# Performance work log

Measured on AMD Instinct MI355X. Metric: run time of the kernel, lower is better.

The kernel has to match this reference:

```python
import jax, jax.numpy as jnp
import numpy as np

RES_DIM = 2048
LEAK_RATE = 0.2
BIAS_SCALE = 0.1


def setup_inputs() -> dict:
    key = jax.random.key(0)
    k_x, k_w, k_b, k_adj = jax.random.split(key, 4)
    x = jax.random.normal(k_x, (RES_DIM, RES_DIM), dtype=jnp.float32)
    # Stand-in for the powerlaw-structured reservoir weight (fixed buffer at runtime);
    # scale so spectral radius is O(1) like normalize_radius_to=1.
    weight = jax.random.normal(k_w, (RES_DIM, RES_DIM), dtype=jnp.float32) / jnp.sqrt(
        jnp.float32(RES_DIM))
    # bias: uniform(-1,1), mean-centered, scaled by bias_scale
    b = jax.random.uniform(k_b, (RES_DIM,), dtype=jnp.float32, minval=-1.0, maxval=1.0)
    bias = (b - b.mean()) * BIAS_SCALE
    # adjacency: random binary 0/1 matrix (np.random.randint(2, size=(D, D)))
    adjacency = (jax.random.uniform(k_adj, (RES_DIM, RES_DIM)) < 0.5).astype(jnp.float32)
    state0 = jnp.zeros((RES_DIM, RES_DIM), dtype=jnp.float32)
    return {"x": x, "weight": weight, "adjacency": adjacency, "bias": bias,
            "state0": state0, "n_steps": 64}


def reference(x, weight, adjacency, bias, state0, n_steps):
    drive = x @ weight + bias  # loop-invariant: precompute once

    def step(state, _):
        y = drive + state @ adjacency
        y = (1.0 - LEAK_RATE) * state + LEAK_RATE * jnp.tanh(y)
        return y, None

    final_state, _ = jax.lax.scan(step, state0, None, length=n_steps)
    return final_state
```

## Files before the change

kernel.cpp:

```cpp
#include <hip/hip_runtime.h>

#define DIM 2048
#define LEAK 0.2f

typedef __bf16 bf16x8 __attribute__((ext_vector_type(8)));
typedef float  f32x4  __attribute__((ext_vector_type(4)));
typedef unsigned int u32x4 __attribute__((ext_vector_type(4)));
typedef int    i32x4  __attribute__((ext_vector_type(4)));

static __device__ __forceinline__ unsigned short f2bf(float f) {
    unsigned int x = __float_as_uint(f);
    return (unsigned short)((x + 0x7fffu + ((x >> 16) & 1u)) >> 16);
}
static __device__ __forceinline__ float bf2f(unsigned short h) {
    return __uint_as_float(((unsigned int)h) << 16);
}

static __device__ __forceinline__ void async16(const void* g, void* s) {
    __builtin_amdgcn_global_load_lds(
        (const __attribute__((address_space(1))) void*)g,
        (__attribute__((address_space(3))) void*)s, 16, 0, 0);
}

static __device__ __forceinline__ bf16x8 ld_bf16_frag(const char* p) {
    union { u32x4 u; bf16x8 v; } cv;
    cv.u = *(const u32x4*)p;
    return cv.v;
}


__global__ __launch_bounds__(256) void split_kernel(
    const float* __restrict__ in,
    unsigned short* __restrict__ hi, unsigned short* __restrict__ lo) {
    int idx = blockIdx.x * 256 + threadIdx.x;
    float4 v = ((const float4*)in)[idx];
    ushort4 h, l;
    h.x = f2bf(v.x); l.x = f2bf(v.x - bf2f(h.x));
    h.y = f2bf(v.y); l.y = f2bf(v.y - bf2f(h.y));
    h.z = f2bf(v.z); l.z = f2bf(v.z - bf2f(h.z));
    h.w = f2bf(v.w); l.w = f2bf(v.w - bf2f(h.w));
    ((ushort4*)hi)[idx] = h;
    ((ushort4*)lo)[idx] = l;
}

__global__ __launch_bounds__(256) void transpose_split(
    const float* __restrict__ in,
    unsigned short* __restrict__ hiT, unsigned short* __restrict__ loT) {
    __shared__ float t[32][33];
    int bx = blockIdx.x, by = blockIdx.y;
    int tx = threadIdx.x & 31, ty4 = (threadIdx.x >> 5) << 2;
#pragma unroll
    for (int i = 0; i < 4; i++)
        t[ty4 + i][tx] = in[(size_t)(by * 32 + ty4 + i) * DIM + bx * 32 + tx];
    __syncthreads();
#pragma unroll
    for (int i = 0; i < 4; i++) {
        float v = t[tx][ty4 + i];
        size_t o = (size_t)(bx * 32 + ty4 + i) * DIM + by * 32 + tx;
        unsigned short h = f2bf(v);
        hiT[o] = h;
        loT[o] = f2bf(v - bf2f(h));
    }
}

__global__ __launch_bounds__(256) void transpose_i8(
    const float* __restrict__ in, signed char* __restrict__ outT) {
    __shared__ float t[32][33];
    int bx = blockIdx.x, by = blockIdx.y;
    int tx = threadIdx.x & 31, ty4 = (threadIdx.x >> 5) << 2;
#pragma unroll
    for (int i = 0; i < 4; i++)
        t[ty4 + i][tx] = in[(size_t)(by * 32 + ty4 + i) * DIM + bx * 32 + tx];
    __syncthreads();
#pragma unroll
    for (int i = 0; i < 4; i++)
        outT[(size_t)(bx * 32 + ty4 + i) * DIM + by * 32 + tx] =
            (signed char)t[tx][ty4 + i];
}

__global__ __launch_bounds__(256) void quant_split(
    const float* __restrict__ in,
    signed char* __restrict__ hi, signed char* __restrict__ lo) {
    int idx = blockIdx.x * 256 + threadIdx.x;
    float4 v = ((const float4*)in)[idx];
    char4 h, l;
    {
        int q = (int)rintf(v.x * 16384.f); q = q > 16383 ? 16383 : (q < -16383 ? -16383 : q);
        h.x = (signed char)(q >> 7); l.x = (signed char)(q & 127);
    }
    {
        int q = (int)rintf(v.y * 16384.f); q = q > 16383 ? 16383 : (q < -16383 ? -16383 : q);
        h.y = (signed char)(q >> 7); l.y = (signed char)(q & 127);
    }
    {
        int q = (int)rintf(v.z * 16384.f); q = q > 16383 ? 16383 : (q < -16383 ? -16383 : q);
        h.z = (signed char)(q >> 7); l.z = (signed char)(q & 127);
    }
    {
        int q = (int)rintf(v.w * 16384.f); q = q > 16383 ? 16383 : (q < -16383 ? -16383 : q);
        h.w = (signed char)(q >> 7); l.w = (signed char)(q & 127);
    }
    ((char4*)hi)[idx] = h;
    ((char4*)lo)[idx] = l;
}

template <int MODE>
__global__ __launch_bounds__(512, 2) void gemm128(
    const unsigned short* __restrict__ Ahi,
    const unsigned short* __restrict__ Alo,
    const unsigned short* __restrict__ BT,
    const float* __restrict__ Cin,
    const float* __restrict__ bias,
    float* __restrict__ Cout) {
    __shared__ alignas(16) char lds[3][49152];

    const int bid = blockIdx.x;
    const int xcd = bid & 7, slot = bid >> 3;
    const int tm = ((xcd >> 1) << 2) + (slot >> 3);
    const int tn = ((xcd & 1) << 3) + (slot & 7);
    const int row0 = tm << 7, col0 = tn << 7;

    const int tid = threadIdx.x;
    const int lane = tid & 63;
    const int quad = lane >> 4, l16 = lane & 15;
    const int wave = tid >> 6;
    const int wm = wave >> 1, wn = wave & 1;

    const unsigned short* a_src[4]; int a_dst[4];
    const unsigned short* b_src[2]; int b_dst[2];
#pragma unroll
    for (int i = 0; i < 4; i++) {
        int s = tid + 512 * i;
        int r = s >> 4, g = (s >> 3) & 1, c = (s & 7) ^ (r & 7);
        a_src[i] = (g ? Alo : Ahi) + (size_t)(row0 + r) * DIM + c * 8;
        a_dst[i] = s * 16;
    }
#pragma unroll
    for (int i = 0; i < 2; i++) {
        int s = tid + 512 * i;
        int r = s >> 3, c = (s & 7) ^ (r & 7);
        b_src[i] = BT + (size_t)(col0 + r) * DIM + c * 8;
        b_dst[i] = s * 16;
    }

    int aoff[2][2], boff[4][2];
#pragma unroll
    for (int i = 0; i < 2; i++)
#pragma unroll
        for (int kk = 0; kk < 2; kk++) {
            const int r = (wm << 5) + (i << 4) + l16;
            const int cs = ((kk << 2) + quad) ^ (r & 7);
            aoff[i][kk] = ((r << 4) + cs) * 16;
        }
#pragma unroll
    for (int j = 0; j < 4; j++)
#pragma unroll
        for (int kk = 0; kk < 2; kk++) {
            const int r = (wn << 6) + (j << 4) + l16;
            const int cs = ((kk << 2) + quad) ^ (r & 7);
            boff[j][kk] = ((r << 3) + cs) * 16;
        }

    f32x4 acc[2][4] = {};

    auto stage6 = [&](char* base, int k0) {
#pragma unroll
        for (int i = 0; i < 4; i++) async16(a_src[i] + k0, base + a_dst[i]);
#pragma unroll
        for (int i = 0; i < 2; i++) async16(b_src[i] + k0, base + 32768 + b_dst[i]);
    };

    stage6(lds[0], 0);
    stage6(lds[1], 64);
    asm volatile("s_waitcnt vmcnt(6)" ::: "memory");

    for (int t = 0; t < 32; ++t) {
        const char* A = lds[t % 3];
        const char* B = A + 32768;

        __builtin_amdgcn_s_barrier();
        __builtin_amdgcn_sched_barrier(0);
        if (t + 2 < 32) stage6(lds[(t + 2) % 3], (t + 2) << 6);

        bf16x8 ah[2][2], al[2][2], bv[4][2];
#pragma unroll
        for (int i = 0; i < 2; i++)
#pragma unroll
            for (int kk = 0; kk < 2; kk++) {
                ah[i][kk] = ld_bf16_frag(A + aoff[i][kk]);
                al[i][kk] = ld_bf16_frag(A + aoff[i][kk] + 128);
            }
#pragma unroll
        for (int j = 0; j < 4; j++)
#pragma unroll
            for (int kk = 0; kk < 2; kk++)
                bv[j][kk] = ld_bf16_frag(B + boff[j][kk]);

        __builtin_amdgcn_s_setprio(1);
#pragma unroll
        for (int i = 0; i < 2; i++)
#pragma unroll
            for (int j = 0; j < 4; j++)
#pragma unroll
                for (int kk = 0; kk < 2; kk++) {
                    acc[i][j] = __builtin_amdgcn_mfma_f32_16x16x32_bf16(ah[i][kk], bv[j][kk], acc[i][j], 0, 0, 0);
                    acc[i][j] = __builtin_amdgcn_mfma_f32_16x16x32_bf16(al[i][kk], bv[j][kk], acc[i][j], 0, 0, 0);
                }
        __builtin_amdgcn_s_setprio(0);

        __builtin_amdgcn_sched_barrier(0);
        if (t < 30)       asm volatile("s_waitcnt vmcnt(6)" ::: "memory");
        else if (t == 30) asm volatile("s_waitcnt vmcnt(0)" ::: "memory");
    }

#pragma unroll
    for (int i = 0; i < 2; i++) {
        const int rb = row0 + (wm << 5) + (i << 4) + (quad << 2);
#pragma unroll
        for (int j = 0; j < 4; j++) {
            const int c = col0 + (wn << 6) + (j << 4) + l16;
#pragma unroll
            for (int g = 0; g < 4; g++) {
                const size_t idx = (size_t)(rb + g) * DIM + c;
                if (MODE == 0) Cout[idx] = acc[i][j][g];
                else           Cout[idx] = Cin[idx] + acc[i][j][g] + bias[c];
            }
        }
    }
}

__global__ __launch_bounds__(512, 2) void step_i8(
    const signed char* __restrict__ Ah,
    const signed char* __restrict__ Al,
    const signed char* __restrict__ BT,
    const float* __restrict__ drive,
    float* __restrict__ out,
    signed char* __restrict__ Oh,
    signed char* __restrict__ Ol,
    int write_f32) {
    __shared__ alignas(16) char lds[3][49152];

    const int bid = blockIdx.x;
    const int xcd = bid & 7, slot = bid >> 3;
    const int tm = ((xcd >> 1) << 2) + (slot >> 3);
    const int tn = ((xcd & 1) << 3) + (slot & 7);
    const int row0 = tm << 7, col0 = tn << 7;

    const int tid = threadIdx.x;
    const int lane = tid & 63;
    const int quad = lane >> 4, l16 = lane & 15;
    const int wave = tid >> 6;
    const int wm = wave >> 1;
    const int wn = wave & 1;

    const signed char* a_src[4]; int a_dst[4];
    const signed char* b_src[2]; int b_dst[2];
#pragma unroll
    for (int i = 0; i < 4; i++) {
        int s = tid + 512 * i;
        int r = s >> 4, g = (s >> 3) & 1, c = (s & 7) ^ (r & 7);
        a_src[i] = (g ? Al : Ah) + (size_t)(row0 + r) * DIM + c * 16;
        a_dst[i] = s * 16;
    }
#pragma unroll
    for (int i = 0; i < 2; i++) {
        int s = tid + 512 * i;
        int r = s >> 3, c = (s & 7) ^ (r & 7);
        b_src[i] = BT + (size_t)(col0 + r) * DIM + c * 16;
        b_dst[i] = s * 16;
    }

    int aoff[2][2], boff[4][2];
#pragma unroll
    for (int i = 0; i < 2; i++)
#pragma unroll
        for (int kk = 0; kk < 2; kk++) {
            const int r = (wm << 5) + (i << 4) + l16;
            const int cs = ((kk << 2) + quad) ^ (r & 7);
            aoff[i][kk] = ((r << 4) + cs) * 16;
        }
#pragma unroll
    for (int j = 0; j < 4; j++)
#pragma unroll
        for (int kk = 0; kk < 2; kk++) {
            const int r = (wn << 6) + (j << 4) + l16;
            const int cs = ((kk << 2) + quad) ^ (r & 7);
            boff[j][kk] = ((r << 3) + cs) * 16;
        }

    i32x4 acch[2][4] = {};
    i32x4 accl[2][4] = {};
    float dreg[2][4][4];

    auto stage6 = [&](char* base, int k0) {
#pragma unroll
        for (int i = 0; i < 4; i++) async16(a_src[i] + k0, base + a_dst[i]);
#pragma unroll
        for (int i = 0; i < 2; i++) async16(b_src[i] + k0, base + 32768 + b_dst[i]);
    };

    stage6(lds[0], 0);
    stage6(lds[1], 128);
    asm volatile("s_waitcnt vmcnt(6)" ::: "memory");

    for (int t = 0; t < 16; ++t) {
        const char* A = lds[t % 3];
        const char* B = A + 32768;

        __builtin_amdgcn_s_barrier();
        __builtin_amdgcn_sched_barrier(0);
        if (t + 2 < 16) stage6(lds[(t + 2) % 3], (t + 2) << 7);

        if (t == 15) {
#pragma unroll
            for (int i = 0; i < 2; i++) {
                const int rb = row0 + (wm << 5) + (i << 4) + (quad << 2);
#pragma unroll
                for (int j = 0; j < 4; j++) {
                    const int c = col0 + (wn << 6) + (j << 4) + l16;
#pragma unroll
                    for (int g = 0; g < 4; g++)
                        dreg[i][j][g] = drive[(size_t)(rb + g) * DIM + c];
                }
            }
        }

        i32x4 ah[2][2], al[2][2], bv[4][2];
#pragma unroll
        for (int i = 0; i < 2; i++)
#pragma unroll
            for (int kk = 0; kk < 2; kk++) {
                ah[i][kk] = *(const i32x4*)(A + aoff[i][kk]);
                al[i][kk] = *(const i32x4*)(A + aoff[i][kk] + 128);
            }
#pragma unroll
        for (int j = 0; j < 4; j++)
#pragma unroll
            for (int kk = 0; kk < 2; kk++)
                bv[j][kk] = *(const i32x4*)(B + boff[j][kk]);

        __builtin_amdgcn_s_setprio(1);
#pragma unroll
        for (int i = 0; i < 2; i++)
#pragma unroll
            for (int j = 0; j < 4; j++)
#pragma unroll
                for (int kk = 0; kk < 2; kk++) {
                    acch[i][j] = __builtin_amdgcn_mfma_i32_16x16x64_i8(ah[i][kk], bv[j][kk], acch[i][j], 0, 0, 0);
                    accl[i][j] = __builtin_amdgcn_mfma_i32_16x16x64_i8(al[i][kk], bv[j][kk], accl[i][j], 0, 0, 0);
                }
        __builtin_amdgcn_s_setprio(0);

        __builtin_amdgcn_sched_barrier(0);
        if (t < 14)       asm volatile("s_waitcnt vmcnt(6)" ::: "memory");
        else if (t == 14) asm volatile("s_waitcnt vmcnt(0)" ::: "memory");
    }

#pragma unroll
    for (int i = 0; i < 2; i++) {
        const int rb = row0 + (wm << 5) + (i << 4) + (quad << 2);
#pragma unroll
        for (int j = 0; j < 4; j++) {
            const int c = col0 + (wn << 6) + (j << 4) + l16;
#pragma unroll
            for (int g = 0; g < 4; g++) {
                const size_t idx = (size_t)(rb + g) * DIM + c;
                int prod = acch[i][j][g] * 128 + accl[i][j][g];
                float y = dreg[i][j][g] + (float)prod * (1.0f / 16384.0f);
                float sold = (float)((int)Ah[idx] * 128 + (int)Al[idx]) * (1.0f / 16384.0f);
                float e = __expf(2.0f * y);
                float th = 1.0f - 2.0f / (e + 1.0f);
                float s = (1.0f - LEAK) * sold + LEAK * th;
                if (write_f32) out[idx] = s;
                int q = (int)rintf(s * 16384.f);
                q = q > 16383 ? 16383 : (q < -16383 ? -16383 : q);
                Oh[idx] = (signed char)(q >> 7);
                Ol[idx] = (signed char)(q & 127);
            }
        }
    }
}

extern "C" void kernel_launch(void* const* d_in, const int* in_sizes, int n_in,
                              void* d_out, int out_size, void* d_ws, size_t ws_size,
                              hipStream_t stream) {
    const float* x    = (const float*)d_in[0];
    const float* wgt  = (const float*)d_in[1];
    const float* adj  = (const float*)d_in[2];
    const float* bias = (const float*)d_in[3];
    const float* st0  = (const float*)d_in[4];
    float* out = (float*)d_out;

    const size_t NE = (size_t)DIM * DIM;
    signed char* adjT = (signed char*)d_ws;
    float* drive = (float*)(adjT + NE);
    unsigned short* bufA = (unsigned short*)(drive + NE);
    unsigned short* bufB = bufA + NE;
    unsigned short* bufC = bufB + NE;
    unsigned short* bufD = bufC + NE;
    signed char* h1 = (signed char*)bufA;
    signed char* l1 = h1 + NE;
    signed char* h2 = l1 + NE;
    signed char* l2 = h2 + NE;

    dim3 blk(256);
    transpose_split<<<dim3(64, 64), blk, 0, stream>>>(wgt, bufC, bufD);
    split_kernel<<<dim3(4096), blk, 0, stream>>>(x, bufA, bufB);
    transpose_i8<<<dim3(64, 64), blk, 0, stream>>>(adj, adjT);

    gemm128<0><<<dim3(256), dim3(512), 0, stream>>>(bufA, bufB, bufC, (const float*)0,
                                                    (const float*)0, drive);
    gemm128<1><<<dim3(256), dim3(512), 0, stream>>>(bufA, bufB, bufD, drive, bias, drive);

    quant_split<<<dim3(4096), blk, 0, stream>>>(st0, h1, l1);

    signed char* hi = h1; signed char* li = l1;
    signed char* ho = h2; signed char* lo = l2;
    for (int t = 0; t < 64; t++) {
        step_i8<<<dim3(256), dim3(512), 0, stream>>>(hi, li, adjT, drive, out,
                                                     ho, lo, (t == 63) ? 1 : 0);
        signed char* th = hi; hi = ho; ho = th;
        signed char* tl = li; li = lo; lo = tl;
    }
}
```

Before: 1.661 ms.

## Load A operand fragments directly into registers instead of staging through LDS

The A tiles (high and low int8 halves) are no longer copied into LDS. Each wave now loads its own A fragments from global memory into double-buffered registers one K-step ahead, and only B is still staged through LDS. This shrinks LDS per block from 3x48KB to 3x16KB, cuts LDS traffic, and may allow higher occupancy. The trade-off is more VGPR pressure, hand-tuned vmcnt counts that mix register and LDS loads, and A rows fetched redundantly by the two waves that share wm.

```diff
diff --git a/kernel.cpp b/kernel.cpp
--- a/kernel.cpp
+++ b/kernel.cpp
@@ -238,7 +238,7 @@
     signed char* __restrict__ Oh,
     signed char* __restrict__ Ol,
     int write_f32) {
-    __shared__ alignas(16) char lds[3][49152];
+    __shared__ alignas(16) char lds[3][16384];
 
     const int bid = blockIdx.x;
     const int xcd = bid & 7, slot = bid >> 3;
@@ -253,15 +253,7 @@
     const int wm = wave >> 1;
     const int wn = wave & 1;
 
-    const signed char* a_src[4]; int a_dst[4];
     const signed char* b_src[2]; int b_dst[2];
-#pragma unroll
-    for (int i = 0; i < 4; i++) {
-        int s = tid + 512 * i;
-        int r = s >> 4, g = (s >> 3) & 1, c = (s & 7) ^ (r & 7);
-        a_src[i] = (g ? Al : Ah) + (size_t)(row0 + r) * DIM + c * 16;
-        a_dst[i] = s * 16;
-    }
 #pragma unroll
     for (int i = 0; i < 2; i++) {
         int s = tid + 512 * i;
@@ -270,15 +262,7 @@
         b_dst[i] = s * 16;
     }
 
-    int aoff[2][2], boff[4][2];
-#pragma unroll
-    for (int i = 0; i < 2; i++)
-#pragma unroll
-        for (int kk = 0; kk < 2; kk++) {
-            const int r = (wm << 5) + (i << 4) + l16;
-            const int cs = ((kk << 2) + quad) ^ (r & 7);
-            aoff[i][kk] = ((r << 4) + cs) * 16;
-        }
+    int boff[4][2];
 #pragma unroll
     for (int j = 0; j < 4; j++)
 #pragma unroll
@@ -288,28 +272,55 @@
             boff[j][kk] = ((r << 3) + cs) * 16;
         }
 
+    const signed char* aHp[2]; const signed char* aLp[2];
+    {
+        const size_t base = (size_t)(row0 + (wm << 5) + l16) * DIM + (quad << 4);
+        aHp[0] = Ah + base;                    aLp[0] = Al + base;
+        aHp[1] = Ah + base + (size_t)16 * DIM; aLp[1] = Al + base + (size_t)16 * DIM;
+    }
+
+    i32x4 areg[2][2][2][2];
     i32x4 acch[2][4] = {};
     i32x4 accl[2][4] = {};
     float dreg[2][4][4];
 
-    auto stage6 = [&](char* base, int k0) {
-#pragma unroll
-        for (int i = 0; i < 4; i++) async16(a_src[i] + k0, base + a_dst[i]);
-#pragma unroll
-        for (int i = 0; i < 2; i++) async16(b_src[i] + k0, base + 32768 + b_dst[i]);
-    };
-
-    stage6(lds[0], 0);
-    stage6(lds[1], 128);
-    asm volatile("s_waitcnt vmcnt(6)" ::: "memory");
-
+#pragma unroll
+    for (int i = 0; i < 2; i++) async16(b_src[i], lds[0] + b_dst[i]);
+#pragma unroll
+    for (int i = 0; i < 2; i++)
+#pragma unroll
+        for (int kk = 0; kk < 2; kk++) {
+            areg[0][i][kk][0] = *(const i32x4*)(aHp[i] + (kk << 6));
+            areg[0][i][kk][1] = *(const i32x4*)(aLp[i] + (kk << 6));
+        }
+#pragma unroll
+    for (int i = 0; i < 2; i++) async16(b_src[i] + 128, lds[1] + b_dst[i]);
+    asm volatile("s_waitcnt vmcnt(10)" ::: "memory");
+
+#pragma unroll
     for (int t = 0; t < 16; ++t) {
-        const char* A = lds[t % 3];
-        const char* B = A + 32768;
+        const char* B = lds[t % 3];
 
         __builtin_amdgcn_s_barrier();
         __builtin_amdgcn_sched_barrier(0);
-        if (t + 2 < 16) stage6(lds[(t + 2) % 3], (t + 2) << 7);
+
+        if (t + 1 < 16) {
+#pragma unroll
+            for (int i = 0; i < 2; i++)
+#pragma unroll
+                for (int kk = 0; kk < 2; kk++) {
+                    areg[(t + 1) & 1][i][kk][0] =
+                        *(const i32x4*)(aHp[i] + ((t + 1) << 7) + (kk << 6));
+                    areg[(t + 1) & 1][i][kk][1] =
+                        *(const i32x4*)(aLp[i] + ((t + 1) << 7) + (kk << 6));
+                }
+        }
+        if (t + 2 < 16) {
+#pragma unroll
+            for (int i = 0; i < 2; i++)
+                async16(b_src[i] + ((t + 2) << 7), lds[(t + 2) % 3] + b_dst[i]);
+        }
+        __builtin_amdgcn_sched_barrier(0);
 
         if (t == 15) {
 #pragma unroll
@@ -325,14 +336,7 @@
             }
         }
 
-        i32x4 ah[2][2], al[2][2], bv[4][2];
-#pragma unroll
-        for (int i = 0; i < 2; i++)
-#pragma unroll
-            for (int kk = 0; kk < 2; kk++) {
-                ah[i][kk] = *(const i32x4*)(A + aoff[i][kk]);
-                al[i][kk] = *(const i32x4*)(A + aoff[i][kk] + 128);
-            }
+        i32x4 bv[4][2];
 #pragma unroll
         for (int j = 0; j < 4; j++)
 #pragma unroll
@@ -346,14 +350,16 @@
             for (int j = 0; j < 4; j++)
 #pragma unroll
                 for (int kk = 0; kk < 2; kk++) {
-                    acch[i][j] = __builtin_amdgcn_mfma_i32_16x16x64_i8(ah[i][kk], bv[j][kk], acch[i][j], 0, 0, 0);
-                    accl[i][j] = __builtin_amdgcn_mfma_i32_16x16x64_i8(al[i][kk], bv[j][kk], accl[i][j], 0, 0, 0);
+                    acch[i][j] = __builtin_amdgcn_mfma_i32_16x16x64_i8(
+                        areg[t & 1][i][kk][0], bv[j][kk], acch[i][j], 0, 0, 0);
+                    accl[i][j] = __builtin_amdgcn_mfma_i32_16x16x64_i8(
+                        areg[t & 1][i][kk][1], bv[j][kk], accl[i][j], 0, 0, 0);
                 }
         __builtin_amdgcn_s_setprio(0);
-
         __builtin_amdgcn_sched_barrier(0);
-        if (t < 14)       asm volatile("s_waitcnt vmcnt(6)" ::: "memory");
-        else if (t == 14) asm volatile("s_waitcnt vmcnt(0)" ::: "memory");
+
+        if (t < 14)       asm volatile("s_waitcnt vmcnt(10)" ::: "memory");
+        else if (t == 14) asm volatile("s_waitcnt vmcnt(8)" ::: "memory");
     }
 
 #pragma unroll
```

After: 3.007 ms. +81.0%, slower.
